# Performance work log

Measured on AMD Instinct MI355X. Metric: run time of the kernel, lower is better.

## Reference

```python
import jax, jax.numpy as jnp
import numpy as np
import math

# ---- static config (matches init_kwargs) ----
LMAX = 2; NC = (LMAX + 1) ** 2        # 9 spherical components
H = 8; DQK = 32; CV = 16; K = 8       # heads, qk dim, value head dim, radial freqs
NTH = 5; NPH = 5; U = NTH * NPH       # 25 sphere directions
N = 2048; C = 256

# ---- Clebsch-Gordan in the real spherical-harmonic basis (numpy, tiny) ----
def _cg(j1, m1, j2, m2, j, m):
    if m1 + m2 != m or j < abs(j1 - j2) or j > j1 + j2:
        return 0.0
    f = math.factorial
    pref = math.sqrt((2 * j + 1) * f(j + j1 - j2) * f(j - j1 + j2) * f(j1 + j2 - j) / f(j1 + j2 + j + 1))
    pref *= math.sqrt(f(j + m) * f(j - m) * f(j1 - m1) * f(j1 + m1) * f(j2 - m2) * f(j2 + m2))
    s = 0.0
    for k in range(0, j1 + j2 - j + 1):
        d = [k, j1 + j2 - j - k, j1 - m1 - k, j2 + m2 - k, j - j2 + m1 + k, j - j1 - m2 + k]
        if min(d) < 0:
            continue
        s += (-1) ** k / (f(d[0]) * f(d[1]) * f(d[2]) * f(d[3]) * f(d[4]) * f(d[5]))
    return pref * s

def _Umat(l):
    u = np.zeros((2 * l + 1, 2 * l + 1), dtype=np.complex128)
    s = 1.0 / math.sqrt(2.0)
    for m in range(-l, l + 1):
        if m > 0:
            u[l + m, l + m] = ((-1) ** m) * s; u[l + m, l - m] = s
        elif m == 0:
            u[l, l] = 1.0
        else:
            u[l + m, l + m] = 1j * s; u[l + m, l - m] = -1j * ((-1) ** m) * s
    return u

def _real_cg(l1, l2, L):
    cgc = np.zeros((2 * l1 + 1, 2 * l2 + 1, 2 * L + 1))
    for i1, m1 in enumerate(range(-l1, l1 + 1)):
        for i2, m2 in enumerate(range(-l2, l2 + 1)):
            for i3, m3 in enumerate(range(-L, L + 1)):
                cgc[i1, i2, i3] = _cg(l1, m1, l2, m2, L, m3)
    r = np.einsum('au,bv,cw,uvw->abc', _Umat(l1), _Umat(l2), np.conj(_Umat(L)), cgc)
    re, im = np.real(r), np.imag(r)
    return re if np.linalg.norm(re) >= np.linalg.norm(im) else im

def _right_reduced():
    off = [0, 1, 4]
    R = np.zeros((NC, NC, NC)); cnt = np.zeros(LMAX + 1)
    for l1 in range(LMAX + 1):
        for l2 in range(LMAX + 1):
            for L in range(abs(l1 - l2), min(l1 + l2, LMAX) + 1):
                R[off[l1]:off[l1] + 2 * l1 + 1, off[l2]:off[l2] + 2 * l2 + 1, off[L]:off[L] + 2 * L + 1] += _real_cg(l1, l2, L)
                cnt[L] += 1
    for L in range(LMAX + 1):
        R[:, :, off[L]:off[L] + 2 * L + 1] /= max(cnt[L], 1.0)
    return R

def _sphere():
    x, w = np.polynomial.legendre.leggauss(NTH)
    phi = 2 * np.pi * np.arange(NPH) / NPH
    ct = np.repeat(x, NPH); wq = np.repeat(w, NPH) * (2 * np.pi / NPH)
    ph = np.tile(phi, NTH); st = np.sqrt(np.maximum(1 - ct * ct, 0.0))
    dirs = np.stack([st * np.cos(ph), st * np.sin(ph), ct], axis=1)
    return dirs, wq

def _ymat(d):
    x, y, z = d[:, 0], d[:, 1], d[:, 2]
    return np.stack([0.282095 * np.ones_like(x), 0.488603 * y, 0.488603 * z, 0.488603 * x,
                     1.092548 * x * y, 1.092548 * y * z, 0.315392 * (3 * z * z - 1),
                     1.092548 * x * z, 0.546274 * (x * x - y * y)], axis=0)  # [9,U]

_DIRS, _WQ = _sphere()
_YW = _ymat(_DIRS) * _WQ[None, :]          # quadrature-weighted Y_l(u): [9,U]
_RRED = _right_reduced()                    # CG coupling ell x lambda -> L<=lmax: [9,9,9]
_LDEG = np.array([0, 1, 1, 1, 2, 2, 2, 2, 2])


def setup_inputs() -> dict:
    key = jax.random.key(0)
    ks = jax.random.split(key, 8)
    node_pos = 3.0 * jax.random.normal(ks[0], (N, 3), dtype=jnp.float32)
    node_feat = jax.random.normal(ks[1], (N, NC, C), dtype=jnp.float32)
    Wq = 0.02 * jax.random.normal(ks[2], (3, C, H * DQK), dtype=jnp.float32)
    Wk = 0.02 * jax.random.normal(ks[3], (3, C, H * DQK), dtype=jnp.float32)
    Wv = jax.random.normal(ks[4], (C, H * CV), dtype=jnp.float32) / math.sqrt(C)
    Wo = jax.random.normal(ks[5], (H * CV, C), dtype=jnp.float32) / math.sqrt(H * CV)
    kappa = jnp.linspace(1.0, 1.4, K, dtype=jnp.float32)
    bias = jnp.exp(-2.0 * (kappa - 1.0) / 0.4)          # low-kappa preference at init
    a = 0.05 * jax.random.normal(ks[6], (3, H, K), dtype=jnp.float32) * bias
    return {"node_pos": node_pos, "node_feat": node_feat, "Wq": Wq, "Wk": Wk,
            "Wv": Wv, "Wo": Wo, "a": a, "kappa": kappa}


def reference(node_pos, node_feat, Wq, Wk, Wv, Wo, a, kappa):
    YW = jnp.asarray(_YW, jnp.float32)
    RRED = jnp.asarray(_RRED, jnp.float32)
    DIRS = jnp.asarray(_DIRS, jnp.float32)
    aE = a[jnp.asarray(_LDEG)]                           # [9,H,K] radial coeffs per ell component

    def so3_to_scalar(x, W):  # invariant q/k projection from irreps
        s = x[:, 0, :] @ W[0]
        s = s + jnp.sqrt(jnp.sum(x[:, 1:4, :] ** 2, axis=1) + 1e-8) @ W[1]
        s = s + jnp.sqrt(jnp.sum(x[:, 4:9, :] ** 2, axis=1) + 1e-8) @ W[2]
        return s

    q = so3_to_scalar(node_feat, Wq).reshape(-1, H, DQK)
    k = so3_to_scalar(node_feat, Wk).reshape(-1, H, DQK)
    qf = jax.nn.elu(q) + 1.0                             # linear-attention feature map
    kf = jax.nn.elu(k) + 1.0
    # value irreps per head: [N,H,Cv,lambda=9]
    v = jnp.einsum('nmc,cf->nmf', node_feat, Wv).reshape(-1, NC, H, CV).transpose(0, 2, 3, 1)

    phase = kappa[None, :, None] * (node_pos @ DIRS.T)[:, None, :]   # [N,K,U]
    cosP = jnp.cos(phase); sinP = jnp.sin(phase)

    acc = jnp.zeros((node_pos.shape[0], H, CV, NC, NC), jnp.float32)  # [N,H,Cv,lambda,ell]
    for kk in range(K):  # small fixed radial-frequency loop
        ck = cosP[:, kk]; sk = sinP[:, kk]
        Yak = jnp.einsum('eu,eh->euh', YW, aE[:, :, kk])              # a_{l,h,k} * w_u * Y_e(u)
        # moments over all nodes (keys x values x phase): [U,H,d,Cv,lambda]
        Mc = jnp.einsum('nhd,nhcl,nu->uhdcl', kf, v, ck)
        Ms = jnp.einsum('nhd,nhcl,nu->uhdcl', kf, v, sk)
        Dc = jnp.einsum('nu,euh->neuh', ck, Yak)
        Ds = jnp.einsum('nu,euh->neuh', sk, Yak)
        acc = acc + jnp.einsum('nhd,uhdcl,neuh->nhcle', qf, Mc, Dc) \
                  + jnp.einsum('nhd,uhdcl,neuh->nhcle', qf, Ms, Ds)
    Z = jnp.einsum('nhd,hd->nh', qf, kf.sum(0)) + 1e-6               # linear-attn normalizer
    acc = acc / Z[:, :, None, None, None]
    # CG coupling ell (x) lambda -> L<=lmax, path-averaged: [N,H,Cv,9]
    outm = jnp.einsum('nhcle,elm->nhcm', acc, RRED)
    out = outm.transpose(0, 3, 1, 2).reshape(-1, NC, H * CV) @ Wo    # [N,9,C]
    return out
```

## Files before the change

### kernel.cpp

```cpp
#include <hip/hip_runtime.h>
#include <cmath>
#include <complex>
#include <algorithm>


typedef _Float16 half8 __attribute__((ext_vector_type(8)));
typedef float float4v __attribute__((ext_vector_type(4)));

namespace {

using cd = std::complex<double>;

static double fct(int n) { double r = 1.0; for (int i = 2; i <= n; ++i) r *= i; return r; }

static double cg_coef(int j1, int m1, int j2, int m2, int j, int m) {
    if (m1 + m2 != m || j < std::abs(j1 - j2) || j > j1 + j2) return 0.0;
    double pref = std::sqrt((2 * j + 1) * fct(j + j1 - j2) * fct(j - j1 + j2) * fct(j1 + j2 - j) / fct(j1 + j2 + j + 1));
    pref *= std::sqrt(fct(j + m) * fct(j - m) * fct(j1 - m1) * fct(j1 + m1) * fct(j2 - m2) * fct(j2 + m2));
    double s = 0.0;
    for (int k = 0; k <= j1 + j2 - j; ++k) {
        int d0 = k, d1 = j1 + j2 - j - k, d2 = j1 - m1 - k, d3 = j2 + m2 - k, d4 = j - j2 + m1 + k, d5 = j - j1 - m2 + k;
        if (d0 < 0 || d1 < 0 || d2 < 0 || d3 < 0 || d4 < 0 || d5 < 0) continue;
        s += ((k & 1) ? -1.0 : 1.0) / (fct(d0) * fct(d1) * fct(d2) * fct(d3) * fct(d4) * fct(d5));
    }
    return pref * s;
}

static void umat(int l, cd u[5][5]) {
    for (int i = 0; i < 5; i++) for (int j = 0; j < 5; j++) u[i][j] = cd(0, 0);
    const double s = 1.0 / std::sqrt(2.0);
    for (int m = -l; m <= l; m++) {
        double sgn = (std::abs(m) & 1) ? -1.0 : 1.0;
        if (m > 0)      { u[l + m][l + m] = cd(sgn * s, 0); u[l + m][l - m] = cd(s, 0); }
        else if (m == 0){ u[l][l] = cd(1, 0); }
        else            { u[l + m][l + m] = cd(0, s);       u[l + m][l - m] = cd(0, -sgn * s); }
    }
}

static void real_cg_f(int l1, int l2, int L, double out[5][5][5]) {
    cd U1[5][5], U2[5][5], UL[5][5];
    umat(l1, U1); umat(l2, U2); umat(L, UL);
    const int n1 = 2 * l1 + 1, n2 = 2 * l2 + 1, n3 = 2 * L + 1;
    double cgt[5][5][5];
    for (int i1 = 0; i1 < n1; i1++) for (int i2 = 0; i2 < n2; i2++) for (int i3 = 0; i3 < n3; i3++)
        cgt[i1][i2][i3] = cg_coef(l1, i1 - l1, l2, i2 - l2, L, i3 - L);
    cd r[5][5][5];
    double nr = 0, ni = 0;
    for (int a1 = 0; a1 < n1; a1++) for (int b = 0; b < n2; b++) for (int c = 0; c < n3; c++) {
        cd acc(0, 0);
        for (int uu = 0; uu < n1; uu++) for (int vv = 0; vv < n2; vv++) for (int w = 0; w < n3; w++) {
            double cval = cgt[uu][vv][w];
            if (cval == 0.0) continue;
            acc += U1[a1][uu] * U2[b][vv] * std::conj(UL[c][w]) * cval;
        }
        r[a1][b][c] = acc;
        nr += acc.real() * acc.real();
        ni += acc.imag() * acc.imag();
    }
    const bool useRe = std::sqrt(nr) >= std::sqrt(ni);
    for (int a1 = 0; a1 < n1; a1++) for (int b = 0; b < n2; b++) for (int c = 0; c < n3; c++)
        out[a1][b][c] = useRe ? r[a1][b][c].real() : r[a1][b][c].imag();
}

static float  h_const[1029];
static float* d_const_g = nullptr;

struct GlobalInit {
    GlobalInit() {
        const double PI = 3.14159265358979323846;
        const double gx[5] = {-0.9061798459386640, -0.5384693101056831, 0.0, 0.5384693101056831, 0.9061798459386640};
        const double gw[5] = { 0.23692688505618908, 0.47862867049936647, 0.5688888888888889, 0.47862867049936647, 0.23692688505618908};
        double YW[9][25], DIRS[25][3];
        for (int u = 0; u < 25; ++u) {
            const int it = u / 5, ip = u % 5;
            const double ct = gx[it], wq = gw[it] * (2.0 * PI / 5.0), ph = 2.0 * PI * ip / 5.0;
            const double st = std::sqrt(std::max(1.0 - ct * ct, 0.0));
            const double x = st * std::cos(ph), y = st * std::sin(ph), z = ct;
            DIRS[u][0] = x; DIRS[u][1] = y; DIRS[u][2] = z;
            double Y[9];
            Y[0] = 0.282095;           Y[1] = 0.488603 * y;      Y[2] = 0.488603 * z;
            Y[3] = 0.488603 * x;       Y[4] = 1.092548 * x * y;  Y[5] = 1.092548 * y * z;
            Y[6] = 0.315392 * (3 * z * z - 1); Y[7] = 1.092548 * x * z; Y[8] = 0.546274 * (x * x - y * y);
            for (int e = 0; e < 9; e++) YW[e][u] = Y[e] * wq;
        }
        double RRED[9][9][9];
        for (int i = 0; i < 9; i++) for (int j = 0; j < 9; j++) for (int k = 0; k < 9; k++) RRED[i][j][k] = 0.0;
        const int off[3] = {0, 1, 4};
        double cnt[3] = {0, 0, 0};
        double rc[5][5][5];
        for (int l1 = 0; l1 <= 2; l1++) for (int l2 = 0; l2 <= 2; l2++) {
            const int Llo = std::abs(l1 - l2), Lhi = std::min(l1 + l2, 2);
            for (int L = Llo; L <= Lhi; L++) {
                real_cg_f(l1, l2, L, rc);
                for (int i1 = 0; i1 < 2 * l1 + 1; i1++)
                    for (int i2 = 0; i2 < 2 * l2 + 1; i2++)
                        for (int i3 = 0; i3 < 2 * L + 1; i3++)
                            RRED[off[l1] + i1][off[l2] + i2][off[L] + i3] += rc[i1][i2][i3];
                cnt[L] += 1.0;
            }
        }
        for (int L = 0; L <= 2; L++) {
            const double dv = std::max(cnt[L], 1.0);
            for (int a1 = 0; a1 < 9; a1++) for (int b = 0; b < 9; b++)
                for (int k = 0; k < 2 * L + 1; k++) RRED[a1][b][off[L] + k] /= dv;
        }
        for (int e = 0; e < 9; e++) for (int u = 0; u < 25; u++) h_const[e * 25 + u] = (float)YW[e][u];
        for (int e = 0; e < 9; e++) for (int l = 0; l < 9; l++) for (int m = 0; m < 9; m++)
            h_const[225 + e * 81 + l * 9 + m] = (float)RRED[e][l][m];
        for (int u = 0; u < 25; u++) for (int ax = 0; ax < 3; ax++) h_const[954 + u * 3 + ax] = (float)DIRS[u][ax];
        if (hipMalloc((void**)&d_const_g, 1029 * sizeof(float)) == hipSuccess)
            hipMemcpy(d_const_g, h_const, 1029 * sizeof(float), hipMemcpyHostToDevice);
    }
} g_init;

}


__global__ void radial_k(const float* __restrict__ feat, float* __restrict__ R) {
    const int n = blockIdx.x, c = threadIdx.x;
    const float* f = feat + (size_t)n * 9 * 256 + c;
    const float f0 = f[0];
    const float a1 = f[256], a2 = f[512], a3 = f[768];
    const float b1 = f[1024], b2 = f[1280], b3 = f[1536], b4 = f[1792], b5 = f[2048];
    const float r1 = sqrtf(a1 * a1 + a2 * a2 + a3 * a3 + 1e-8f);
    const float r2 = sqrtf(b1 * b1 + b2 * b2 + b3 * b3 + b4 * b4 + b5 * b5 + 1e-8f);
    float* o = R + (size_t)n * 768 + c;
    o[0] = f0; o[256] = r1; o[512] = r2;
}

__global__ __launch_bounds__(256) void qk_gemm_k(const float* __restrict__ A,
                                                 const float* __restrict__ Wq,
                                                 const float* __restrict__ Wk,
                                                 float* __restrict__ qf,
                                                 _Float16* __restrict__ kfA) {
    __shared__ __align__(16) _Float16 Af[64 * 40];
    __shared__ __align__(16) _Float16 Bf[64 * 40];
    const int tid = threadIdx.x;
    const int w = tid >> 6, lane = tid & 63;
    const int l15 = lane & 15, quad = lane >> 4;
    const bool isK = blockIdx.x >= 4;
    const int cb = (blockIdx.x & 3) * 64;
    const int rb = blockIdx.y * 64;
    const float* B = isK ? Wk : Wq;
    const int N = 256, Kd = 768;
    const int sr = tid >> 2, sq = tid & 3;

    float4v acc[4];
#pragma unroll
    for (int s = 0; s < 4; s++) acc[s] = float4v{0.f, 0.f, 0.f, 0.f};

    for (int k0 = 0; k0 < Kd; k0 += 32) {
        __syncthreads();
        {
            const float* Ap = A + (size_t)(rb + sr) * Kd + k0 + sq * 8;
            const float4 a0 = *(const float4*)(Ap);
            const float4 a1 = *(const float4*)(Ap + 4);
            half8 hv;
            hv[0] = (_Float16)a0.x; hv[1] = (_Float16)a0.y; hv[2] = (_Float16)a0.z; hv[3] = (_Float16)a0.w;
            hv[4] = (_Float16)a1.x; hv[5] = (_Float16)a1.y; hv[6] = (_Float16)a1.z; hv[7] = (_Float16)a1.w;
            *(half8*)&Af[sr * 40 + sq * 8] = hv;
        }
        {
            const float* Bp = B + (size_t)(k0 + sq * 8) * N + cb + sr;
            half8 hv;
#pragma unroll
            for (int i = 0; i < 8; i++) hv[i] = (_Float16)Bp[(size_t)i * N];
            *(half8*)&Bf[sr * 40 + sq * 8] = hv;
        }
        __syncthreads();
        const half8 af = *(const half8*)&Af[(w * 16 + l15) * 40 + quad * 8];
#pragma unroll
        for (int s = 0; s < 4; s++) {
            const half8 bf = *(const half8*)&Bf[(s * 16 + l15) * 40 + quad * 8];
            acc[s] = __builtin_amdgcn_mfma_f32_16x16x32_f16(af, bf, acc[s], 0, 0, 0);
        }
    }
#pragma unroll
    for (int s = 0; s < 4; s++) {
#pragma unroll
        for (int r = 0; r < 4; r++) {
            const int row = rb + w * 16 + quad * 4 + r;
            const int col = cb + s * 16 + l15;
            float val = acc[s][r];
            val = (val > 0.f ? val : expf(val) - 1.f) + 1.f;
            if (isK) {
                const int hh = col >> 5, dd = col & 31, tt = dd >> 4, ll = dd & 15;
                kfA[(size_t)hh * 65536 + (size_t)(row >> 5) * 1024 + tt * 512 + ll * 32 + (row & 31)] = (_Float16)val;
            } else {
                qf[(size_t)row * 256 + col] = val;
            }
        }
    }
}

__global__ __launch_bounds__(256) void mfma_gemm16_k(const float* __restrict__ A, const float* __restrict__ B,
                                                     float* __restrict__ Cv, int M, int N, int Kd, int mode,
                                                     const float* __restrict__ rZ) {
    __shared__ __align__(16) _Float16 Af[64 * 40];
    __shared__ __align__(16) _Float16 Bf[64 * 40];
    const int tid = threadIdx.x;
    const int w = tid >> 6, lane = tid & 63;
    const int l15 = lane & 15, quad = lane >> 4;
    const int rb = blockIdx.y * 64, cb = blockIdx.x * 64;
    const int sr = tid >> 2, sq = tid & 3;

    float4v acc[4];
#pragma unroll
    for (int s = 0; s < 4; s++) acc[s] = float4v{0.f, 0.f, 0.f, 0.f};

    for (int k0 = 0; k0 < Kd; k0 += 32) {
        __syncthreads();
        {
            const float* Ap = A + (size_t)(rb + sr) * Kd + k0 + sq * 8;
            float4 a0, a1;
            if (mode == 4) {
                const float4 p00 = *(const float4*)(Ap);
                const float4 p01 = *(const float4*)(Ap + 4);
                const float4 p10 = *(const float4*)(Ap + 2359296);
                const float4 p11 = *(const float4*)(Ap + 2359296 + 4);
                const float4 p20 = *(const float4*)(Ap + 4718592);
                const float4 p21 = *(const float4*)(Ap + 4718592 + 4);
                const float4 p30 = *(const float4*)(Ap + 7077888);
                const float4 p31 = *(const float4*)(Ap + 7077888 + 4);
                const int n = (rb + sr) / 9;
                const int hh = (k0 + sq * 8) >> 4;
                const float rz = rZ[n * 8 + hh];
                a0.x = (p00.x + p10.x + p20.x + p30.x) * rz;
                a0.y = (p00.y + p10.y + p20.y + p30.y) * rz;
                a0.z = (p00.z + p10.z + p20.z + p30.z) * rz;
                a0.w = (p00.w + p10.w + p20.w + p30.w) * rz;
                a1.x = (p01.x + p11.x + p21.x + p31.x) * rz;
                a1.y = (p01.y + p11.y + p21.y + p31.y) * rz;
                a1.z = (p01.z + p11.z + p21.z + p31.z) * rz;
                a1.w = (p01.w + p11.w + p21.w + p31.w) * rz;
            } else {
                a0 = *(const float4*)(Ap);
                a1 = *(const float4*)(Ap + 4);
            }
            half8 hv;
            hv[0] = (_Float16)a0.x; hv[1] = (_Float16)a0.y; hv[2] = (_Float16)a0.z; hv[3] = (_Float16)a0.w;
            hv[4] = (_Float16)a1.x; hv[5] = (_Float16)a1.y; hv[6] = (_Float16)a1.z; hv[7] = (_Float16)a1.w;
            *(half8*)&Af[sr * 40 + sq * 8] = hv;
        }
        {
            const float* Bp = B + (size_t)(k0 + sq * 8) * N + cb + sr;
            half8 hv;
#pragma unroll
            for (int i = 0; i < 8; i++) hv[i] = (_Float16)Bp[(size_t)i * N];
            *(half8*)&Bf[sr * 40 + sq * 8] = hv;
        }
        __syncthreads();
        const half8 af = *(const half8*)&Af[(w * 16 + l15) * 40 + quad * 8];
#pragma unroll
        for (int s = 0; s < 4; s++) {
            const half8 bf = *(const half8*)&Bf[(s * 16 + l15) * 40 + quad * 8];
            acc[s] = __builtin_amdgcn_mfma_f32_16x16x32_f16(af, bf, acc[s], 0, 0, 0);
        }
    }
#pragma unroll
    for (int s = 0; s < 4; s++) {
#pragma unroll
        for (int r = 0; r < 4; r++) {
            const int row = rb + w * 16 + quad * 4 + r;
            const int col = cb + s * 16 + l15;
            float val = acc[s][r];
            if (mode == 2) {
                const int n = row / 9, l = row - n * 9, hq = col >> 4, cvq = col & 15;
                _Float16* o = (_Float16*)Cv;
                o[((size_t)hq * 144 + cvq * 9 + l) * 2048 + n] = (_Float16)val;
            } else {
                Cv[(size_t)row * N + col] = val;
            }
        }
    }
}

__global__ void trig_k(const float* __restrict__ pos, const float* __restrict__ kappa,
                       const float* __restrict__ cst, _Float16* __restrict__ trigA) {
    const int n = blockIdx.x, t = threadIdx.x;
    const size_t base = (size_t)(n >> 5) * 16384 + (n & 31);
    if (t < 200) {
        const int kq = t / 25, u = t - kq * 25;
        const float* dirs = cst + 954;
        const float ph = kappa[kq] * (pos[n * 3] * dirs[u * 3] + pos[n * 3 + 1] * dirs[u * 3 + 1] + pos[n * 3 + 2] * dirs[u * 3 + 2]);
        float s, c;
        sincosf(ph, &s, &c);
        const int kkut = (kq * 25 + u) * 2;
        trigA[base + (size_t)kkut * 32] = (_Float16)c;
        trigA[base + (size_t)(kkut + 1) * 32] = (_Float16)s;
    } else {
        const int kkut = 400 + (t - 200) * 2;
        trigA[base + (size_t)kkut * 32] = (_Float16)0.f;
        trigA[base + (size_t)(kkut + 1) * 32] = (_Float16)0.f;
    }
}

__global__ void ksumT_k(const _Float16* __restrict__ kfA, float* __restrict__ ksum) {
    const int b = blockIdx.x;
    const int h = b >> 5, d = b & 31, t = d >> 4, l15 = d & 15;
    const int i = threadIdx.x;
    const half8 v = *(const half8*)(kfA + (size_t)h * 65536 + (size_t)(i >> 2) * 1024 + t * 512 + l15 * 32 + (i & 3) * 8);
    float s = 0.f;
#pragma unroll
    for (int k = 0; k < 8; k++) s += (float)v[k];
#pragma unroll
    for (int off = 32; off > 0; off >>= 1) s += __shfl_down(s, off, 64);
    __shared__ float red[4];
    if ((i & 63) == 0) red[i >> 6] = s;
    __syncthreads();
    if (i == 0) ksum[b] = red[0] + red[1] + red[2] + red[3];
}

__global__ void zg_k(const float* __restrict__ qf, const float* __restrict__ ksum, float* __restrict__ rz,
                     const float* __restrict__ a, const float* __restrict__ cst, float* __restrict__ G) {
    if (blockIdx.x < 64) {
        const int idx = blockIdx.x * 256 + threadIdx.x;
        const int n = idx >> 3, h = idx & 7;
        float s = 0.f;
#pragma unroll
        for (int d = 0; d < 32; d++) s += qf[(size_t)n * 256 + h * 32 + d] * ksum[h * 32 + d];
        rz[idx] = 1.0f / (s + 1e-6f);
    } else {
        const int b = blockIdx.x - 64;
        const int kk = b & 7, h = b >> 3;
        __shared__ float ae[9];
        if (threadIdx.x < 9) {
            const int ldeg[9] = {0, 1, 1, 1, 2, 2, 2, 2, 2};
            ae[threadIdx.x] = a[ldeg[threadIdx.x] * 64 + h * 8 + kk];
        }
        __syncthreads();
        const float* yw = cst;
        const float* rred = cst + 225;
        for (int i = threadIdx.x; i < 25 * 81; i += 256) {
            const int u = i / 81, lm = i - u * 81;
            float s = 0.f;
#pragma unroll
            for (int e = 0; e < 9; e++) s += ae[e] * yw[e * 25 + u] * rred[e * 81 + lm];
            G[((size_t)(kk * 8 + h) * 25 + u) * 81 + lm] = s;
        }
    }
}

__global__ __launch_bounds__(256, 3) void multipole_mm_k(const _Float16* __restrict__ trigA,
                                                         const _Float16* __restrict__ kfA,
                                                         const _Float16* __restrict__ v16T,
                                                         _Float16* __restrict__ M16) {
    const int h   = blockIdx.x;
    const int tid = threadIdx.x;
    const int w = tid >> 6, lane = tid & 63;
    const int l15 = lane & 15, quad = lane >> 4;
    const int cb  = blockIdx.y * 512 + w * 128;
    const int cl0 = cb >> 5;
    const int r0  = blockIdx.z * 32;

    __shared__ __align__(16) _Float16 sb[2][20][512];

    float4v acc[2][8];
#pragma unroll
    for (int rt = 0; rt < 2; rt++)
#pragma unroll
        for (int s = 0; s < 8; s++) acc[rt][s] = float4v{0.f, 0.f, 0.f, 0.f};

    const _Float16* afg0 = trigA + (size_t)(r0 + l15) * 32 + quad * 8;
    const _Float16* afg1 = afg0 + 512;
    const _Float16* kqg0 = kfA + (size_t)h * 65536 + (size_t)l15 * 32 + quad * 8;
    const _Float16* kqg1 = kqg0 + 512;
    const int vs = lane >> 4, vc = (lane >> 2) & 3, vg = lane & 3;
    const _Float16* vqg = v16T + (size_t)(h * 144 + cl0 + vc) * 2048 + vs * 32 + vg * 8;

    half8 g0, g1, g2, g3, g4;

#define GATHER(nbr_) { \
        const size_t t5 = (size_t)((nbr_) >> 5) + w; \
        g0 = *(const half8*)(afg0 + t5 * 16384); \
        g1 = *(const half8*)(afg1 + t5 * 16384); \
        g2 = *(const half8*)(kqg0 + t5 * 1024); \
        g3 = *(const half8*)(kqg1 + t5 * 1024); \
        g4 = *(const half8*)(vqg + (nbr_)); }

#define DSWRITE(b_) { \
        *(half8*)&sb[b_][w * 4 + 0][lane * 8] = g0; \
        *(half8*)&sb[b_][w * 4 + 1][lane * 8] = g1; \
        *(half8*)&sb[b_][w * 4 + 2][lane * 8] = g2; \
        *(half8*)&sb[b_][w * 4 + 3][lane * 8] = g3; \
        *(half8*)&sb[b_][16 + w][lane * 8] = g4; }

#define STEP(s_) { \
        const half8 af0 = *(const half8*)&sb[cur][(s_) * 4 + 0][lane * 8]; \
        const half8 af1 = *(const half8*)&sb[cur][(s_) * 4 + 1][lane * 8]; \
        const half8 kq0 = *(const half8*)&sb[cur][(s_) * 4 + 2][lane * 8]; \
        const half8 kq1 = *(const half8*)&sb[cur][(s_) * 4 + 3][lane * 8]; \
        _Pragma("unroll") \
        for (int c = 0; c < 4; c++) { \
            const half8 vq = *(const half8*)&sb[cur][16 + w][((s_) * 4 + c) * 32 + quad * 8]; \
            const half8 b0 = kq0 * vq; \
            const half8 b1 = kq1 * vq; \
            acc[0][2 * c]     = __builtin_amdgcn_mfma_f32_16x16x32_f16(af0, b0, acc[0][2 * c],     0, 0, 0); \
            acc[0][2 * c + 1] = __builtin_amdgcn_mfma_f32_16x16x32_f16(af0, b1, acc[0][2 * c + 1], 0, 0, 0); \
            acc[1][2 * c]     = __builtin_amdgcn_mfma_f32_16x16x32_f16(af1, b0, acc[1][2 * c],     0, 0, 0); \
            acc[1][2 * c + 1] = __builtin_amdgcn_mfma_f32_16x16x32_f16(af1, b1, acc[1][2 * c + 1], 0, 0, 0); \
        } }

    int cur = 0;
    GATHER(0)
    DSWRITE(0)
    __syncthreads();
#pragma unroll 1
    for (int r = 0; r < 16; ++r) {
        if (r < 15) GATHER((r + 1) * 128)
        STEP(0)
        STEP(1)
        STEP(2)
        STEP(3)
        if (r < 15) DSWRITE(cur ^ 1)
        __syncthreads();
        cur ^= 1;
    }

#undef GATHER
#undef DSWRITE
#undef STEP

#pragma unroll
    for (int rt = 0; rt < 2; rt++)
#pragma unroll
        for (int c = 0; c < 4; c++)
#pragma unroll
            for (int half = 0; half < 2; half++)
#pragma unroll
                for (int r = 0; r < 4; r++) {
                    const int row = r0 + rt * 16 + quad * 4 + r;
                    const int col = cb + c * 32 + half * 16 + l15;
                    M16[((size_t)row * 8 + h) * 4608 + col] = (_Float16)acc[rt][c * 2 + half][r];
                }
}

__global__ __launch_bounds__(256) void fold_k(const _Float16* __restrict__ Mv, const float* __restrict__ G,
                                              _Float16* __restrict__ MG) {
    const int kt = blockIdx.x, h = blockIdx.y;
    const int tid = threadIdx.x;
    __shared__ float ms[144 * 33];
    __shared__ float gs[81];
    const _Float16* src = Mv + ((size_t)kt * 8 + h) * 4608;
    for (int i = tid; i < 4608; i += 256) {
        const int cl = i >> 5, d = i & 31;
        ms[cl * 33 + d] = (float)src[i];
    }
    const int kk = kt / 50, u = (kt >> 1) % 25;
    if (tid < 81) gs[tid] = G[(((size_t)kk * 8 + h) * 25 + u) * 81 + tid];
    __syncthreads();
    _Float16* dst = MG + ((size_t)kt * 8 + h) * 4608;
    for (int i = tid; i < 4608; i += 256) {
        const int ct = i >> 9, quad = (i >> 7) & 3, l15 = (i >> 3) & 15, j = i & 7;
        const int d = quad * 8 + j;
        const int cm = ct * 16 + l15, c = cm / 9, m = cm - c * 9;
        float s = 0.f;
#pragma unroll
        for (int l = 0; l < 9; l++) s += ms[(c * 9 + l) * 33 + d] * gs[l * 9 + m];
        dst[i] = (_Float16)s;
    }
}

__global__ __launch_bounds__(256, 2) void mm_local_k(const float* __restrict__ qf, const _Float16* __restrict__ trigA,
                                                     const _Float16* __restrict__ MG, float* __restrict__ outp) {
    const int combo = blockIdx.y * 8 + blockIdx.x;
    const int h = combo >> 2;
    const int slice = combo & 3;
    const int n0 = blockIdx.z * 128;
    const int tid = threadIdx.x;
    const int w = tid >> 6, lane = tid & 63;
    const int l15 = lane & 15, quad = lane >> 4;

    __shared__ __align__(16) _Float16 sb[2][4][4608];

    const int nbase = n0 + w * 32;
    half8 qfr16[2];
#pragma unroll
    for (int rt = 0; rt < 2; rt++) {
        const int n = nbase + rt * 16 + l15;
        const float* qp = qf + (size_t)n * 256 + h * 32 + quad * 8;
#pragma unroll
        for (int j = 0; j < 8; j++) qfr16[rt][j] = (_Float16)qp[j];
    }
    float4v acc[2][9];
#pragma unroll
    for (int rt = 0; rt < 2; rt++)
#pragma unroll
        for (int ct = 0; ct < 9; ct++) acc[rt][ct] = float4v{0.f, 0.f, 0.f, 0.f};

    const int kt0 = slice * 100;
    const _Float16* mg0 = MG + (((size_t)kt0 * 8 + h) * 4608) + lane * 8;
    const _Float16* trg0 = trigA + (size_t)(nbase >> 5) * 16384 + (size_t)kt0 * 32 + l15;

#define STAGE(b_, r_) { \
        const _Float16* src = mg0 + (size_t)((r_) * 4 + w) * 8 * 4608; \
        _Float16* dstl = &sb[b_][w][0]; \
        _Pragma("unroll") \
        for (int i = 0; i < 9; i++) \
            __builtin_amdgcn_global_load_lds( \
                (const __attribute__((address_space(1))) void*)(src + i * 512), \
                (__attribute__((address_space(3))) void*)(dstl + i * 512), 16, 0, 0); }

    _Float16 t0[4], t1[4], u0[4], u1[4];
    int cur = 0;
    STAGE(0, 0)
#pragma unroll
    for (int kl = 0; kl < 4; kl++) { t0[kl] = trg0[kl * 32]; t1[kl] = trg0[kl * 32 + 16]; }
    __syncthreads();

#pragma unroll 1
    for (int r = 0; r < 25; ++r) {
        if (r < 24) {
            STAGE(cur ^ 1, r + 1)
#pragma unroll
            for (int kl = 0; kl < 4; kl++) {
                u0[kl] = trg0[((size_t)((r + 1) * 4 + kl)) * 32];
                u1[kl] = trg0[((size_t)((r + 1) * 4 + kl)) * 32 + 16];
            }
        }
#pragma unroll
        for (int kl = 0; kl < 4; kl++) {
            half8 tvv0, tvv1;
#pragma unroll
            for (int j = 0; j < 8; j++) { tvv0[j] = t0[kl]; tvv1[j] = t1[kl]; }
            const half8 af0 = tvv0 * qfr16[0];
            const half8 af1 = tvv1 * qfr16[1];
#pragma unroll
            for (int ct = 0; ct < 9; ct++) {
                const half8 b = *(const half8*)&sb[cur][kl][ct * 512 + quad * 128 + l15 * 8];
                acc[0][ct] = __builtin_amdgcn_mfma_f32_16x16x32_f16(af0, b, acc[0][ct], 0, 0, 0);
                acc[1][ct] = __builtin_amdgcn_mfma_f32_16x16x32_f16(af1, b, acc[1][ct], 0, 0, 0);
            }
        }
        __syncthreads();
        cur ^= 1;
#pragma unroll
        for (int kl = 0; kl < 4; kl++) { t0[kl] = u0[kl]; t1[kl] = u1[kl]; }
    }
#undef STAGE

    float* ebp = (float*)sb;
    float* dst = outp + (size_t)slice * 2359296;
    const int g4 = lane >> 2, sub = lane & 3;
#pragma unroll
    for (int rt = 0; rt < 2; rt++) {
        __syncthreads();
#pragma unroll
        for (int ct = 0; ct < 9; ct++) {
            const int cm = ct * 16 + l15;
            const int c = cm / 9, m = cm - c * 9;
#pragma unroll
            for (int r = 0; r < 4; r++)
                ebp[(size_t)(w * 16 + quad * 4 + r) * 148 + m * 16 + c] = acc[rt][ct][r];
        }
        __syncthreads();
#pragma unroll
        for (int s = 0; s < 9; s++) {
            const int li = s * 16 + g4;
            const int nl = li / 9, m = li - nl * 9;
            const float4 v4 = *(const float4*)&ebp[(size_t)(w * 16 + nl) * 148 + m * 16 + sub * 4];
            const int n = nbase + rt * 16 + nl;
            *(float4*)&dst[((size_t)n * 9 + m) * 128 + h * 16 + sub * 4] = v4;
        }
    }
}

extern "C" void kernel_launch(void* const* d_in, const int* in_sizes, int n_in,
                              void* d_out, int out_size, void* d_ws, size_t ws_size,
                              hipStream_t stream) {
    const float* pos  = (const float*)d_in[0];
    const float* feat = (const float*)d_in[1];
    const float* Wq   = (const float*)d_in[2];
    const float* Wk   = (const float*)d_in[3];
    const float* Wv   = (const float*)d_in[4];
    const float* Wo   = (const float*)d_in[5];
    const float* a    = (const float*)d_in[6];
    const float* kap  = (const float*)d_in[7];
    float* out = (float*)d_out;
    float* ws = (float*)d_ws;

    float* qf    = ws;
    float* kfAF  = qf + 524288;
    float* vTF   = kfAF + 262144;
    float* trigF = vTF + 1179648;
    float* ksum  = trigF + 524288;
    float* rz    = ksum + 256;
    float* G     = rz + 16384;
    float* M16F  = G + 129600;
    float* regX  = M16F + 9437184;
    float* R     = regX;
    float* outp  = M16F;
    _Float16* trigA = (_Float16*)trigF;
    _Float16* kfA   = (_Float16*)kfAF;
    _Float16* v16T  = (_Float16*)vTF;
    _Float16* M16   = (_Float16*)M16F;
    _Float16* MG16  = (_Float16*)regX;

    const float* cst = d_const_g;

    hipLaunchKernelGGL(radial_k, dim3(2048), dim3(256), 0, stream, feat, R);
    hipLaunchKernelGGL(qk_gemm_k, dim3(8, 32), dim3(256), 0, stream, R, Wq, Wk, qf, kfA);
    hipLaunchKernelGGL(mfma_gemm16_k, dim3(2, 288), dim3(256), 0, stream, feat, Wv, vTF, 18432, 128, 256, 2, rz);
    hipLaunchKernelGGL(trig_k, dim3(2048), dim3(256), 0, stream, pos, kap, cst, trigA);
    hipLaunchKernelGGL(ksumT_k, dim3(256), dim3(256), 0, stream, kfA, ksum);
    hipLaunchKernelGGL(zg_k, dim3(128), dim3(256), 0, stream, qf, ksum, rz, a, cst, G);
    hipLaunchKernelGGL(multipole_mm_k, dim3(8, 9, 13), dim3(256), 0, stream, trigA, kfA, v16T, M16);
    hipLaunchKernelGGL(fold_k, dim3(400, 8), dim3(256), 0, stream, M16, G, MG16);
    hipLaunchKernelGGL(mm_local_k, dim3(8, 4, 16), dim3(256), 0, stream, qf, trigA, MG16, outp);
    hipLaunchKernelGGL(mfma_gemm16_k, dim3(4, 288), dim3(256), 0, stream, outp, Wo, out, 18432, 256, 128, 4, rz);
}
```

Before: 320.3 us.

## Double rows per wave in mm_local and store partial outputs as fp16

The mm_local kernel now gives each wave 64 nodes instead of 32, so every staged MG tile from LDS is reused by twice as many MFMAs. The grid is halved and the occupancy hint drops to one block per CU. The four-slice partial output is now written in fp16 instead of fp32, and the output GEMM reads it as fp16. This halves the partial-buffer traffic at the cost of some precision and more register pressure.

```diff
diff --git a/kernel.cpp b/kernel.cpp
--- a/kernel.cpp
+++ b/kernel.cpp
@@ -5,6 +5,7 @@
 
 
 typedef _Float16 half8 __attribute__((ext_vector_type(8)));
+typedef _Float16 half4v __attribute__((ext_vector_type(4)));
 typedef float float4v __attribute__((ext_vector_type(4)));
 
 namespace {
@@ -210,33 +211,24 @@
 
     for (int k0 = 0; k0 < Kd; k0 += 32) {
         __syncthreads();
-        {
+        if (mode == 4) {
+            const _Float16* Ap16 = (const _Float16*)A + (size_t)(rb + sr) * Kd + k0 + sq * 8;
+            const half8 p0 = *(const half8*)(Ap16);
+            const half8 p1 = *(const half8*)(Ap16 + 2359296);
+            const half8 p2 = *(const half8*)(Ap16 + 4718592);
+            const half8 p3 = *(const half8*)(Ap16 + 7077888);
+            const int n = (rb + sr) / 9;
+            const int hh = (k0 + sq * 8) >> 4;
+            const float rz = rZ[n * 8 + hh];
+            half8 hv;
+#pragma unroll
+            for (int i = 0; i < 8; i++)
+                hv[i] = (_Float16)(((float)p0[i] + (float)p1[i] + (float)p2[i] + (float)p3[i]) * rz);
+            *(half8*)&Af[sr * 40 + sq * 8] = hv;
+        } else {
             const float* Ap = A + (size_t)(rb + sr) * Kd + k0 + sq * 8;
-            float4 a0, a1;
-            if (mode == 4) {
-                const float4 p00 = *(const float4*)(Ap);
-                const float4 p01 = *(const float4*)(Ap + 4);
-                const float4 p10 = *(const float4*)(Ap + 2359296);
-                const float4 p11 = *(const float4*)(Ap + 2359296 + 4);
-                const float4 p20 = *(const float4*)(Ap + 4718592);
-                const float4 p21 = *(const float4*)(Ap + 4718592 + 4);
-                const float4 p30 = *(const float4*)(Ap + 7077888);
-                const float4 p31 = *(const float4*)(Ap + 7077888 + 4);
-                const int n = (rb + sr) / 9;
-                const int hh = (k0 + sq * 8) >> 4;
-                const float rz = rZ[n * 8 + hh];
-                a0.x = (p00.x + p10.x + p20.x + p30.x) * rz;
-                a0.y = (p00.y + p10.y + p20.y + p30.y) * rz;
-                a0.z = (p00.z + p10.z + p20.z + p30.z) * rz;
-                a0.w = (p00.w + p10.w + p20.w + p30.w) * rz;
-                a1.x = (p01.x + p11.x + p21.x + p31.x) * rz;
-                a1.y = (p01.y + p11.y + p21.y + p31.y) * rz;
-                a1.z = (p01.z + p11.z + p21.z + p31.z) * rz;
-                a1.w = (p01.w + p11.w + p21.w + p31.w) * rz;
-            } else {
-                a0 = *(const float4*)(Ap);
-                a1 = *(const float4*)(Ap + 4);
-            }
+            const float4 a0 = *(const float4*)(Ap);
+            const float4 a1 = *(const float4*)(Ap + 4);
             half8 hv;
             hv[0] = (_Float16)a0.x; hv[1] = (_Float16)a0.y; hv[2] = (_Float16)a0.z; hv[3] = (_Float16)a0.w;
             hv[4] = (_Float16)a1.x; hv[5] = (_Float16)a1.y; hv[6] = (_Float16)a1.z; hv[7] = (_Float16)a1.w;
@@ -461,30 +453,30 @@
     }
 }
 
-__global__ __launch_bounds__(256, 2) void mm_local_k(const float* __restrict__ qf, const _Float16* __restrict__ trigA,
-                                                     const _Float16* __restrict__ MG, float* __restrict__ outp) {
+__global__ __launch_bounds__(256, 1) void mm_local_k(const float* __restrict__ qf, const _Float16* __restrict__ trigA,
+                                                     const _Float16* __restrict__ MG, _Float16* __restrict__ outp) {
     const int combo = blockIdx.y * 8 + blockIdx.x;
     const int h = combo >> 2;
     const int slice = combo & 3;
-    const int n0 = blockIdx.z * 128;
+    const int n0 = blockIdx.z * 256;
     const int tid = threadIdx.x;
     const int w = tid >> 6, lane = tid & 63;
     const int l15 = lane & 15, quad = lane >> 4;
 
     __shared__ __align__(16) _Float16 sb[2][4][4608];
 
-    const int nbase = n0 + w * 32;
-    half8 qfr16[2];
-#pragma unroll
-    for (int rt = 0; rt < 2; rt++) {
+    const int nbase = n0 + w * 64;
+    half8 qfr16[4];
+#pragma unroll
+    for (int rt = 0; rt < 4; rt++) {
         const int n = nbase + rt * 16 + l15;
         const float* qp = qf + (size_t)n * 256 + h * 32 + quad * 8;
 #pragma unroll
         for (int j = 0; j < 8; j++) qfr16[rt][j] = (_Float16)qp[j];
     }
-    float4v acc[2][9];
-#pragma unroll
-    for (int rt = 0; rt < 2; rt++)
+    float4v acc[4][9];
+#pragma unroll
+    for (int rt = 0; rt < 4; rt++)
 #pragma unroll
         for (int ct = 0; ct < 9; ct++) acc[rt][ct] = float4v{0.f, 0.f, 0.f, 0.f};
 
@@ -501,11 +493,14 @@
                 (const __attribute__((address_space(1))) void*)(src + i * 512), \
                 (__attribute__((address_space(3))) void*)(dstl + i * 512), 16, 0, 0); }
 
-    _Float16 t0[4], t1[4], u0[4], u1[4];
+    _Float16 ta[4], tb[4], tc[4], td[4], ua[4], ub[4], uc[4], ud[4];
     int cur = 0;
     STAGE(0, 0)
 #pragma unroll
-    for (int kl = 0; kl < 4; kl++) { t0[kl] = trg0[kl * 32]; t1[kl] = trg0[kl * 32 + 16]; }
+    for (int kl = 0; kl < 4; kl++) {
+        ta[kl] = trg0[kl * 32];           tb[kl] = trg0[kl * 32 + 16];
+        tc[kl] = trg0[16384 + kl * 32];   td[kl] = trg0[16384 + kl * 32 + 16];
+    }
     __syncthreads();
 
 #pragma unroll 1
@@ -514,36 +509,41 @@
             STAGE(cur ^ 1, r + 1)
 #pragma unroll
             for (int kl = 0; kl < 4; kl++) {
-                u0[kl] = trg0[((size_t)((r + 1) * 4 + kl)) * 32];
-                u1[kl] = trg0[((size_t)((r + 1) * 4 + kl)) * 32 + 16];
+                const size_t o = (size_t)((r + 1) * 4 + kl) * 32;
+                ua[kl] = trg0[o];           ub[kl] = trg0[o + 16];
+                uc[kl] = trg0[16384 + o];   ud[kl] = trg0[16384 + o + 16];
             }
         }
 #pragma unroll
         for (int kl = 0; kl < 4; kl++) {
-            half8 tvv0, tvv1;
-#pragma unroll
-            for (int j = 0; j < 8; j++) { tvv0[j] = t0[kl]; tvv1[j] = t1[kl]; }
-            const half8 af0 = tvv0 * qfr16[0];
-            const half8 af1 = tvv1 * qfr16[1];
+            half8 tv0, tv1, tv2, tv3;
+#pragma unroll
+            for (int j = 0; j < 8; j++) { tv0[j] = ta[kl]; tv1[j] = tb[kl]; tv2[j] = tc[kl]; tv3[j] = td[kl]; }
+            const half8 af0 = tv0 * qfr16[0];
+            const half8 af1 = tv1 * qfr16[1];
+            const half8 af2 = tv2 * qfr16[2];
+            const half8 af3 = tv3 * qfr16[3];
 #pragma unroll
             for (int ct = 0; ct < 9; ct++) {
                 const half8 b = *(const half8*)&sb[cur][kl][ct * 512 + quad * 128 + l15 * 8];
                 acc[0][ct] = __builtin_amdgcn_mfma_f32_16x16x32_f16(af0, b, acc[0][ct], 0, 0, 0);
                 acc[1][ct] = __builtin_amdgcn_mfma_f32_16x16x32_f16(af1, b, acc[1][ct], 0, 0, 0);
+                acc[2][ct] = __builtin_amdgcn_mfma_f32_16x16x32_f16(af2, b, acc[2][ct], 0, 0, 0);
+                acc[3][ct] = __builtin_amdgcn_mfma_f32_16x16x32_f16(af3, b, acc[3][ct], 0, 0, 0);
             }
         }
         __syncthreads();
         cur ^= 1;
 #pragma unroll
-        for (int kl = 0; kl < 4; kl++) { t0[kl] = u0[kl]; t1[kl] = u1[kl]; }
+        for (int kl = 0; kl < 4; kl++) { ta[kl] = ua[kl]; tb[kl] = ub[kl]; tc[kl] = uc[kl]; td[kl] = ud[kl]; }
     }
 #undef STAGE
 
     float* ebp = (float*)sb;
-    float* dst = outp + (size_t)slice * 2359296;
+    _Float16* dst = outp + (size_t)slice * 2359296;
     const int g4 = lane >> 2, sub = lane & 3;
 #pragma unroll
-    for (int rt = 0; rt < 2; rt++) {
+    for (int rt = 0; rt < 4; rt++) {
         __syncthreads();
 #pragma unroll
         for (int ct = 0; ct < 9; ct++) {
@@ -560,7 +560,9 @@
             const int nl = li / 9, m = li - nl * 9;
             const float4 v4 = *(const float4*)&ebp[(size_t)(w * 16 + nl) * 148 + m * 16 + sub * 4];
             const int n = nbase + rt * 16 + nl;
-            *(float4*)&dst[((size_t)n * 9 + m) * 128 + h * 16 + sub * 4] = v4;
+            half4v hv;
+            hv[0] = (_Float16)v4.x; hv[1] = (_Float16)v4.y; hv[2] = (_Float16)v4.z; hv[3] = (_Float16)v4.w;
+            *(half4v*)&dst[((size_t)n * 9 + m) * 128 + h * 16 + sub * 4] = hv;
         }
     }
 }
@@ -589,12 +591,12 @@
     float* M16F  = G + 129600;
     float* regX  = M16F + 9437184;
     float* R     = regX;
-    float* outp  = M16F;
     _Float16* trigA = (_Float16*)trigF;
     _Float16* kfA   = (_Float16*)kfAF;
     _Float16* v16T  = (_Float16*)vTF;
     _Float16* M16   = (_Float16*)M16F;
     _Float16* MG16  = (_Float16*)regX;
+    _Float16* outp16 = (_Float16*)M16F;
 
     const float* cst = d_const_g;
 
@@ -606,6 +608,6 @@
     hipLaunchKernelGGL(zg_k, dim3(128), dim3(256), 0, stream, qf, ksum, rz, a, cst, G);
     hipLaunchKernelGGL(multipole_mm_k, dim3(8, 9, 13), dim3(256), 0, stream, trigA, kfA, v16T, M16);
     hipLaunchKernelGGL(fold_k, dim3(400, 8), dim3(256), 0, stream, M16, G, MG16);
-    hipLaunchKernelGGL(mm_local_k, dim3(8, 4, 16), dim3(256), 0, stream, qf, trigA, MG16, outp);
-    hipLaunchKernelGGL(mfma_gemm16_k, dim3(4, 288), dim3(256), 0, stream, outp, Wo, out, 18432, 256, 128, 4, rz);
-}
+    hipLaunchKernelGGL(mm_local_k, dim3(8, 4, 8), dim3(256), 0, stream, qf, trigA, MG16, outp16);
+    hipLaunchKernelGGL(mfma_gemm16_k, dim3(4, 288), dim3(256), 0, stream, (const float*)outp16, Wo, out, 18432, 256, 128, 4, rz);
+}
```

New measurement: 320.1 us. No clear change (-0.1%).
